# Performance work log

Measured on AMD Instinct MI355X. Metric: run time of the kernel, lower is better.

The kernel has to match this reference:

```python
import jax, jax.numpy as jnp
import numpy as np
import math

N, E, G = 10000, 100000, 500
HID, H = 128, 4
C = HID                      # out_channels per head (PyG TransformerConv)
NFREQ, NSPACE = 10, 3
EDIM = 2 * NFREQ * NSPACE    # 60 = dis_emb.dim
LAT, DIS = 6, 3
IN_DIM = HID + LAT + DIS     # 137
EPS = 1e-5


def _lin_init(k, fan_in, shape):
    b = 1.0 / math.sqrt(fan_in)
    return jax.random.uniform(k, shape, jnp.float32, -b, b)


def setup_inputs() -> dict:
    key = jax.random.key(0)
    ks = jax.random.split(key, 12)
    return dict(
        node_features=jax.random.normal(ks[0], (N, HID), jnp.float32),
        frac_coords=jax.random.uniform(ks[1], (N, DIS), jnp.float32),
        lattice_feats=jax.random.normal(ks[2], (G, LAT), jnp.float32),
        edge_index=jax.random.randint(ks[3], (2, E), 0, N),
        node2graph=jnp.sort(jax.random.randint(ks[4], (N,), 0, G)),
        frac_diff=jax.random.normal(ks[5], (E, DIS), jnp.float32) * 0.1,
        ln_gamma=jnp.ones((HID,), jnp.float32),
        ln_beta=jnp.zeros((HID,), jnp.float32),
        Wq=_lin_init(ks[6], IN_DIM, (IN_DIM, H * C)), bq=jnp.zeros((H * C,), jnp.float32),
        Wk=_lin_init(ks[7], IN_DIM, (IN_DIM, H * C)), bk=jnp.zeros((H * C,), jnp.float32),
        Wv=_lin_init(ks[8], IN_DIM, (IN_DIM, H * C)), bv=jnp.zeros((H * C,), jnp.float32),
        We=_lin_init(ks[9], EDIM, (EDIM, H * C)),
        Wskip=_lin_init(ks[10], IN_DIM, (IN_DIM, C)), bskip=jnp.zeros((C,), jnp.float32),
    )


def _sinusoids(frac_diff):
    # SinusoidsEmbedding: emb = x[...,None]*2*pi*arange(F); cat(sin, cos); detached
    freqs = 2.0 * jnp.pi * jnp.arange(NFREQ, dtype=jnp.float32)    # [F]
    emb = frac_diff[:, :, None] * freqs[None, None, :]             # [E,3,F]
    emb = emb.reshape(-1, NSPACE * NFREQ)                          # [E,30]
    return jnp.concatenate([jnp.sin(emb), jnp.cos(emb)], axis=-1)  # [E,60]


def _segment_softmax(scores, idx, num_segments):
    # softmax over variable-size neighborhoods grouped by target node idx
    m = jax.ops.segment_max(scores, idx, num_segments=num_segments)
    ex = jnp.exp(scores - m[idx])
    s = jax.ops.segment_sum(ex, idx, num_segments=num_segments)
    return ex / (s[idx] + 1e-16)


def reference(node_features, frac_coords, lattice_feats, edge_index, node2graph,
              frac_diff, ln_gamma, ln_beta, Wq, bq, Wk, bk, Wv, bv, We, Wskip, bskip):
    edge_emb = jax.lax.stop_gradient(_sinusoids(frac_diff))  # .detach() in original
    node_input = node_features
    # LayerNorm (biased variance, torch default)
    mu = node_features.mean(-1, keepdims=True)
    var = node_features.var(-1, keepdims=True)
    h = (node_features - mu) * jax.lax.rsqrt(var + EPS) * ln_gamma + ln_beta
    # gather per-graph lattice features to nodes, concat
    lat = lattice_feats.reshape(-1, LAT)[node2graph]                # [N,6]
    x = jnp.concatenate([h, lat, frac_coords], axis=1)              # [N,137]

    q = (x @ Wq + bq).reshape(N, H, C)
    k = (x @ Wk + bk).reshape(N, H, C)
    v = (x @ Wv + bv).reshape(N, H, C)
    e = (edge_emb @ We).reshape(E, H, C)                            # lin_edge (no bias)

    src, dst = edge_index[0], edge_index[1]  # message flows src -> dst (PyG default)
    k_e = k[src] + e                                                # [E,H,C]
    alpha = (q[dst] * k_e).sum(-1) / math.sqrt(C)                   # [E,H]
    alpha = _segment_softmax(alpha, dst, N)
    msg = (v[src] + e) * alpha[:, :, None]                          # [E,H,C]
    out = jax.ops.segment_sum(msg, dst, num_segments=N)             # [N,H,C]
    out = out.mean(axis=1)                                          # concat=False -> head mean
    out = out + (x @ Wskip + bskip)                                 # root skip connection
    return node_input + jax.nn.silu(out)
```

## Files before the change

kernel.cpp:

```cpp
#include <hip/hip_runtime.h>
#include <math.h>

#define N_NODES 10000
#define N_EDGES 100000
#define HIDDEN  128
#define NHEAD   4
#define CHAN    128
#define IN_DIM  137
#define KPAD    160
#define NCOLS   1904
#define NPAD    1920
#define LATD    6
#define DISD    3

#define PREP_BLOCKS 2500
#define TRANS_TILES 26
#define WQE_BLOCKS  150
#define WEBT_BLOCKS 128

#define SCAT_BLOCKS ((N_EDGES + 255) / 256)
#define GEMM_BX 15
#define GEMM_BY ((N_NODES + 63) / 64)
#define NR16    628
#define FRAG_STRIDE (5 * 64 * 8)

typedef __attribute__((ext_vector_type(8))) short short8v;
typedef __attribute__((ext_vector_type(4))) float float4v;
typedef __attribute__((ext_vector_type(2))) float float2v;

__device__ inline unsigned short f2bf(float f) {
    unsigned u = __float_as_uint(f);
    unsigned r = 0x7fffu + ((u >> 16) & 1u);
    return (unsigned short)((u + r) >> 16);
}
__device__ inline float bf2f(unsigned short u) {
    return __uint_as_float(((unsigned)u) << 16);
}
__device__ inline size_t frag_off(int grp16, int ks, int lane) {
    return (((size_t)grp16 * 5 + ks) * 64 + lane) * 8;
}
__device__ inline size_t frag_elem(int grp16, int lr, int k) {
    const int ks = k >> 5, g = (k >> 3) & 3, e = k & 7;
    return frag_off(grp16, ks, g * 16 + lr) + e;
}

__global__ __launch_bounds__(256) void prep_weights_kernel(
    const float* __restrict__ nf, const float* __restrict__ frac,
    const float* __restrict__ lat, const int* __restrict__ n2g,
    const float* __restrict__ gamma, const float* __restrict__ beta,
    const float* __restrict__ Wq, const float* __restrict__ bq,
    const float* __restrict__ Wk, const float* __restrict__ bk,
    const float* __restrict__ Wv, const float* __restrict__ bv,
    const float* __restrict__ Wsk, const float* __restrict__ bsk,
    const float* __restrict__ We,
    unsigned short* __restrict__ xfrag, int* __restrict__ hist,
    unsigned short* __restrict__ wfrag, float* __restrict__ bias_all,
    unsigned short* __restrict__ webt)
{
    __shared__ __align__(16) unsigned short Tlds[64 * 168];
    const int tid = threadIdx.x;

    if (blockIdx.x < PREP_BLOCKS) {
        int wave = tid >> 6;
        int lane = tid & 63;
        int n = blockIdx.x * 4 + wave;
        if (n >= N_NODES) return;

        float v0 = nf[n * HIDDEN + lane];
        float v1 = nf[n * HIDDEN + 64 + lane];
        float s  = v0 + v1;
        float sq = v0 * v0 + v1 * v1;
        #pragma unroll
        for (int m = 1; m < 64; m <<= 1) {
            s  += __shfl_xor(s, m);
            sq += __shfl_xor(sq, m);
        }
        float mean = s * (1.0f / 128.0f);
        float var  = sq * (1.0f / 128.0f) - mean * mean;
        float inv  = rsqrtf(var + 1e-5f);

        const int r16 = n >> 4, lr = n & 15;
        xfrag[frag_elem(r16, lr, lane)] =
            f2bf((v0 - mean) * inv * gamma[lane] + beta[lane]);
        xfrag[frag_elem(r16, lr, 64 + lane)] =
            f2bf((v1 - mean) * inv * gamma[64 + lane] + beta[64 + lane]);
        if (lane < LATD)
            xfrag[frag_elem(r16, lr, HIDDEN + lane)] = f2bf(lat[n2g[n] * LATD + lane]);
        if (lane < DISD)
            xfrag[frag_elem(r16, lr, HIDDEN + LATD + lane)] = f2bf(frac[n * DISD + lane]);
        if (lane >= 41)
            xfrag[frag_elem(r16, lr, 96 + lane)] = 0;
        if (lane == 0) hist[n] = 0;
    } else if (blockIdx.x < PREP_BLOCKS + TRANS_TILES) {
        const int n0 = (blockIdx.x - PREP_BLOCKS) * 64;
        for (int i = tid; i < 160 * 64; i += 256) {
            const int k = i >> 6, n = i & 63;
            const int col = n0 + n;
            float val = 0.0f;
            if (k < IN_DIM) {
                if (col < 512)        val = Wq[(size_t)k * 512 + col];
                else if (col < 1024)  val = Wk[(size_t)k * 512 + (col - 512)];
                else if (col < 1536)  val = Wv[(size_t)k * 512 + (col - 1024)];
                else                  val = Wsk[(size_t)k * 128 + (col - 1536)];
            }
            Tlds[n * 168 + k] = f2bf(val);
        }
        __syncthreads();
        for (int i = tid; i < 4 * 5 * 64; i += 256) {
            const int lane = i & 63;
            const int ks   = (i >> 6) % 5;
            const int c16l = i / (5 * 64);
            const int lr = lane & 15, g = lane >> 4;
            const int lcol = c16l * 16 + lr;
            const int k0 = ks * 32 + g * 8;
            const short8v v = *reinterpret_cast<const short8v*>(&Tlds[lcol * 168 + k0]);
            *reinterpret_cast<short8v*>(
                &wfrag[frag_off((n0 >> 4) + c16l, ks, lane)]) = v;
        }
        if (tid < 64) {
            const int col = n0 + tid;
            float b;
            if (col < 512)        b = bq[col];
            else if (col < 1024)  b = bk[col - 512];
            else if (col < 1536)  b = bv[col - 1024];
            else                  b = bsk[col - 1536];
            bias_all[col] = b;
        }
    } else if (blockIdx.x < PREP_BLOCKS + TRANS_TILES + WQE_BLOCKS) {
        int idx = (blockIdx.x - PREP_BLOCKS - TRANS_TILES) * 256 + tid;
        if (idx >= 240 * KPAD) return;
        int hj = idx / KPAD, k = idx % KPAD;
        int h = hj / 60, j = hj % 60;
        float s = 0.0f;
        if (k < IN_DIM) {
            #pragma unroll 4
            for (int c = 0; c < 128; ++c)
                s += Wq[(size_t)k * 512 + h * 128 + c] * We[(size_t)j * 512 + h * 128 + c];
        }
        const int col = 1664 + hj;
        wfrag[frag_elem(col >> 4, col & 15, k)] = f2bf(s);
        if (k == KPAD - 1) {
            float b = 0.0f;
            #pragma unroll 4
            for (int c = 0; c < 128; ++c)
                b += bq[h * 128 + c] * We[(size_t)j * 512 + h * 128 + c];
            bias_all[col] = b;
        }
    } else {
        int g = (blockIdx.x - PREP_BLOCKS - TRANS_TILES - WQE_BLOCKS) * 256 + tid;
        if (g >= 4 * 128 * 64) return;
        int h = g >> 13, c = (g >> 6) & 127, j = g & 63;
        float v = (j < 60) ? We[(size_t)j * 512 + h * 128 + c] : 0.0f;
        webt[g] = f2bf(v);
    }
}

__global__ __launch_bounds__(256) void hist_kernel(
    const int* __restrict__ eidx, int* __restrict__ hist)
{
    int e = blockIdx.x * 256 + threadIdx.x;
    if (e < N_EDGES) atomicAdd(&hist[eidx[N_EDGES + e]], 1);
}

__global__ __launch_bounds__(1024) void scan_kernel(
    const int* __restrict__ hist, int* __restrict__ offsets, int* __restrict__ cursor)
{
    __shared__ int part[1024];
    const int t = threadIdx.x;
    const int base = t * 10;
    int loc[10];
    int s = 0;
    #pragma unroll
    for (int i = 0; i < 10; ++i) {
        int v = (base + i < N_NODES) ? hist[base + i] : 0;
        loc[i] = s; s += v;
    }
    part[t] = s;
    __syncthreads();
    for (int off = 1; off < 1024; off <<= 1) {
        int v = (t >= off) ? part[t - off] : 0;
        __syncthreads();
        part[t] += v;
        __syncthreads();
    }
    int pre = (t > 0) ? part[t - 1] : 0;
    #pragma unroll
    for (int i = 0; i < 10; ++i)
        if (base + i < N_NODES) {
            offsets[base + i] = pre + loc[i];
            cursor[base + i]  = pre + loc[i];
        }
    if (t == 1023) offsets[N_NODES] = part[1023];
}

__global__ __launch_bounds__(256, 2) void gemm_scatter_kernel(
    const unsigned short* __restrict__ xfrag, const unsigned short* __restrict__ wfrag,
    const float* __restrict__ bias_all,
    const int* __restrict__ eidx, const float* __restrict__ fdiff,
    int* __restrict__ cursor, int* __restrict__ sorted_src,
    float* __restrict__ sorted_fd,
    float* __restrict__ sq, unsigned short* __restrict__ qbuf,
    unsigned char* __restrict__ kvb)
{
    if (blockIdx.x < SCAT_BLOCKS) {
        int e = blockIdx.x * 256 + threadIdx.x;
        if (e >= N_EDGES) return;
        int src = eidx[e];
        int dst = eidx[N_EDGES + e];
        int pos = atomicAdd(&cursor[dst], 1);
        sorted_src[pos] = src;
        sorted_fd[pos * 3 + 0] = fdiff[e * 3 + 0];
        sorted_fd[pos * 3 + 1] = fdiff[e * 3 + 1];
        sorted_fd[pos * 3 + 2] = fdiff[e * 3 + 2];
        return;
    }

    const int bx   = blockIdx.x - SCAT_BLOCKS;
    const int row0 = (bx / GEMM_BX) * 64;
    const int col0 = (bx % GEMM_BX) * 128;
    const int tid  = threadIdx.x;
    const int l    = tid & 63;
    const int wid  = tid >> 6;
    const int wr   = (wid >> 1) * 32;
    const int wc   = (wid & 1) * 64;
    const int lr   = l & 15;
    const int r16  = (row0 + wr) >> 4;
    const int c16  = (col0 + wc) >> 4;

    short8v a[2][5], b[4][5];
    #pragma unroll
    for (int ks = 0; ks < 5; ++ks) {
        #pragma unroll
        for (int t = 0; t < 2; ++t)
            a[t][ks] = *reinterpret_cast<const short8v*>(
                &xfrag[frag_off(r16 + t, ks, l)]);
        #pragma unroll
        for (int t = 0; t < 4; ++t)
            b[t][ks] = *reinterpret_cast<const short8v*>(
                &wfrag[frag_off(c16 + t, ks, l)]);
    }

    float4v acc[2][4];
    #pragma unroll
    for (int tr = 0; tr < 2; ++tr)
        #pragma unroll
        for (int tc = 0; tc < 4; ++tc)
            acc[tr][tc] = (float4v){0.0f, 0.0f, 0.0f, 0.0f};

    #pragma unroll
    for (int ks = 0; ks < 5; ++ks)
        #pragma unroll
        for (int tr = 0; tr < 2; ++tr)
            #pragma unroll
            for (int tc = 0; tc < 4; ++tc)
                acc[tr][tc] = __builtin_amdgcn_mfma_f32_16x16x32_bf16(
                    a[tr][ks], b[tc][ks], acc[tr][tc], 0, 0, 0);

    #pragma unroll
    for (int tr = 0; tr < 2; ++tr) {
        #pragma unroll
        for (int tc = 0; tc < 4; ++tc) {
            const int col  = col0 + wc + tc * 16 + lr;
            const float bias = bias_all[col];
            #pragma unroll
            for (int j = 0; j < 4; ++j) {
                const int row = row0 + wr + tr * 16 + (l >> 4) * 4 + j;
                if (row < N_NODES) {
                    float val = acc[tr][tc][j] + bias;
                    if (col < 512) {
                        qbuf[(size_t)row * 512 + col] = f2bf(val);
                    } else if (col < 1024) {
                        const int h = (col - 512) >> 7, ck = (col - 512) & 127;
                        int p = __builtin_amdgcn_cvt_pk_fp8_f32(val, val, 0, false);
                        kvb[((size_t)row * 4 + h) * 256 + ck] = (unsigned char)(p & 0xFF);
                    } else if (col < 1536) {
                        const int h = (col - 1024) >> 7, cv = (col - 1024) & 127;
                        int p = __builtin_amdgcn_cvt_pk_fp8_f32(val, val, 0, false);
                        kvb[((size_t)row * 4 + h) * 256 + 128 + cv] = (unsigned char)(p & 0xFF);
                    } else if (col < 1664) {
                        sq[(size_t)row * 384 + (col - 1536)] = val;
                    } else if (col < NCOLS) {
                        sq[(size_t)row * 384 + 128 + (col - 1664)] = val;
                    }
                }
            }
        }
    }
}

__global__ __launch_bounds__(256) void gather_kernel(
    const float* __restrict__ sq, const unsigned short* __restrict__ qbuf,
    const unsigned char* __restrict__ kvb,
    const int* __restrict__ offsets, const int* __restrict__ sorted_src,
    const float* __restrict__ sorted_fd,
    float* __restrict__ avbuf, unsigned short* __restrict__ aggbuf,
    float* __restrict__ sumwbuf)
{
    const int n    = blockIdx.x;
    const int h    = threadIdx.x >> 6;
    const int l    = threadIdx.x & 63;
    const int hl   = l & 31;
    const int half = l >> 5;
    const float TWO_PI = 6.283185307179586f;
    const float scale  = 0.08838834764831845f;

    const ushort4 qv = *reinterpret_cast<const ushort4*>(
        &qbuf[(size_t)n * 512 + h * 128 + 4 * hl]);
    const float q4x = bf2f(qv.x), q4y = bf2f(qv.y);
    const float q4z = bf2f(qv.z), q4w = bf2f(qv.w);
    const float qe_a = sq[(size_t)n * 384 + 128 + h * 60 + hl];
    const bool  v2ok = (hl < 28);
    const float qe_b = v2ok ? sq[(size_t)n * 384 + 128 + h * 60 + hl + 32] : 0.0f;

    const int   jj1  = (hl < 30) ? hl : hl - 30;
    const int   sd1  = jj1 / 10;
    const float fc1  = TWO_PI * (float)(jj1 % 10);
    const bool  sin1 = (hl < 30);
    const int   jj2  = hl + 2;
    const int   sd2  = v2ok ? (jj2 / 10) : 0;
    const float fc2  = v2ok ? TWO_PI * (float)(jj2 % 10) : 0.0f;

    float ax = 0.f, ay = 0.f, az = 0.f, aw = 0.f;
    float agg1 = 0.f, agg2 = 0.f, sumw = 0.f;
    const int e0 = offsets[n], e1 = offsets[n + 1];

    for (int base = e0; base < e1; base += 4) {
        const int eA = base + half;
        const int eB = base + half + 2;
        const bool okA = (eA < e1), okB = (eB < e1);
        const int iA = okA ? eA : e0;
        const int iB = okB ? eB : e0;
        const int srcA = sorted_src[iA];
        const int srcB = sorted_src[iB];
        const float fdA1 = sorted_fd[iA * 3 + sd1];
        const float fdA2 = sorted_fd[iA * 3 + sd2];
        const float fdB1 = sorted_fd[iB * 3 + sd1];
        const float fdB2 = sorted_fd[iB * 3 + sd2];
        const unsigned char* pA = kvb + ((size_t)srcA * 4 + h) * 256;
        const unsigned char* pB = kvb + ((size_t)srcB * 4 + h) * 256;
        const unsigned kAu = *reinterpret_cast<const unsigned*>(pA + 4 * hl);
        const unsigned vAu = *reinterpret_cast<const unsigned*>(pA + 128 + 4 * hl);
        const unsigned kBu = *reinterpret_cast<const unsigned*>(pB + 4 * hl);
        const unsigned vBu = *reinterpret_cast<const unsigned*>(pB + 128 + 4 * hl);

        const float eA1 = sin1 ? __sinf(fdA1 * fc1) : __cosf(fdA1 * fc1);
        const float eA2 = __cosf(fdA2 * fc2);
        const float eB1 = sin1 ? __sinf(fdB1 * fc1) : __cosf(fdB1 * fc1);
        const float eB2 = __cosf(fdB2 * fc2);

        const float2v kA01 = __builtin_amdgcn_cvt_pk_f32_fp8(kAu, false);
        const float2v kA23 = __builtin_amdgcn_cvt_pk_f32_fp8(kAu, true);
        const float2v kB01 = __builtin_amdgcn_cvt_pk_f32_fp8(kBu, false);
        const float2v kB23 = __builtin_amdgcn_cvt_pk_f32_fp8(kBu, true);

        float pAs = q4x * kA01[0] + q4y * kA01[1]
                  + q4z * kA23[0] + q4w * kA23[1]
                  + eA1 * qe_a + eA2 * qe_b;
        float pBs = q4x * kB01[0] + q4y * kB01[1]
                  + q4z * kB23[0] + q4w * kB23[1]
                  + eB1 * qe_a + eB2 * qe_b;
        #pragma unroll
        for (int m = 1; m <= 16; m <<= 1) {
            pAs += __shfl_xor(pAs, m);
            pBs += __shfl_xor(pBs, m);
        }
        const float wA = okA ? __expf(pAs * scale) : 0.0f;
        const float wB = okB ? __expf(pBs * scale) : 0.0f;
        sumw += wA + wB;

        const float2v vA01 = __builtin_amdgcn_cvt_pk_f32_fp8(vAu, false);
        const float2v vA23 = __builtin_amdgcn_cvt_pk_f32_fp8(vAu, true);
        const float2v vB01 = __builtin_amdgcn_cvt_pk_f32_fp8(vBu, false);
        const float2v vB23 = __builtin_amdgcn_cvt_pk_f32_fp8(vBu, true);
        ax += wA * vA01[0] + wB * vB01[0];
        ay += wA * vA01[1] + wB * vB01[1];
        az += wA * vA23[0] + wB * vB23[0];
        aw += wA * vA23[1] + wB * vB23[1];
        agg1 += wA * eA1 + wB * eB1;
        if (v2ok) agg2 += wA * eA2 + wB * eB2;
    }

    sumw += __shfl_xor(sumw, 32);
    ax += __shfl_xor(ax, 32);  ay += __shfl_xor(ay, 32);
    az += __shfl_xor(az, 32);  aw += __shfl_xor(aw, 32);
    agg1 += __shfl_xor(agg1, 32);
    agg2 += __shfl_xor(agg2, 32);

    if (half == 0) {
        float4 r;
        r.x = ax; r.y = ay; r.z = az; r.w = aw;
        *reinterpret_cast<float4*>(&avbuf[(size_t)n * 512 + h * 128 + 4 * hl]) = r;
        aggbuf[n * 256 + h * 64 + hl]      = f2bf(agg1);
        aggbuf[n * 256 + h * 64 + 32 + hl] = f2bf(agg2);
        if (hl == 0) sumwbuf[n * 4 + h] = sumw;
    }
}

__global__ __launch_bounds__(256) void corrfin_kernel(
    const unsigned short* __restrict__ webt, const unsigned short* __restrict__ aggbuf,
    const float* __restrict__ avbuf, const float* __restrict__ sumwbuf,
    const float* __restrict__ sq, const float* __restrict__ nf,
    float* __restrict__ out)
{
    const int node0 = blockIdx.x * 64;
    const int tid = threadIdx.x;
    const int l   = tid & 63;
    const int w   = tid >> 6;
    const int lr  = l & 15;
    const int lk  = (l >> 4) * 8;
    const int nbase = node0 + w * 16;

    float4v acc[4][8];
    #pragma unroll
    for (int h = 0; h < 4; ++h)
        #pragma unroll
        for (int nn = 0; nn < 8; ++nn)
            acc[h][nn] = (float4v){0.0f, 0.0f, 0.0f, 0.0f};

    const int arow = (nbase + lr < N_NODES) ? (nbase + lr) : 0;
    #pragma unroll
    for (int h = 0; h < 4; ++h) {
        #pragma unroll
        for (int ks = 0; ks < 2; ++ks) {
            const short8v a = *reinterpret_cast<const short8v*>(
                &aggbuf[(size_t)arow * 256 + h * 64 + ks * 32 + lk]);
            #pragma unroll
            for (int nn = 0; nn < 8; ++nn) {
                const short8v b = *reinterpret_cast<const short8v*>(
                    &webt[(size_t)(h * 128 + nn * 16 + lr) * 64 + ks * 32 + lk]);
                acc[h][nn] = __builtin_amdgcn_mfma_f32_16x16x32_bf16(a, b, acc[h][nn], 0, 0, 0);
            }
        }
    }

    float inv_sw[4][4];
    #pragma unroll
    for (int j = 0; j < 4; ++j) {
        const int node = nbase + (l >> 4) * 4 + j;
        const int nrd  = (node < N_NODES) ? node : 0;
        #pragma unroll
        for (int h = 0; h < 4; ++h)
            inv_sw[j][h] = 1.0f / (sumwbuf[nrd * 4 + h] + 1e-16f);
    }

    #pragma unroll
    for (int nn = 0; nn < 8; ++nn) {
        const int col = nn * 16 + lr;
        #pragma unroll
        for (int j = 0; j < 4; ++j) {
            const int node = nbase + (l >> 4) * 4 + j;
            if (node < N_NODES) {
                float z = 0.0f;
                #pragma unroll
                for (int h = 0; h < 4; ++h)
                    z += (avbuf[(size_t)node * 512 + h * 128 + col] + acc[h][nn][j])
                         * inv_sw[j][h];
                z = 0.25f * z + sq[(size_t)node * 384 + col];
                float si = z / (1.0f + __expf(-z));
                out[node * CHAN + col] = nf[node * CHAN + col] + si;
            }
        }
    }
}

extern "C" void kernel_launch(void* const* d_in, const int* in_sizes, int n_in,
                              void* d_out, int out_size, void* d_ws, size_t ws_size,
                              hipStream_t stream)
{
    const float* nf    = (const float*)d_in[0];
    const float* frac  = (const float*)d_in[1];
    const float* lat   = (const float*)d_in[2];
    const int*   eidx  = (const int*)  d_in[3];
    const int*   n2g   = (const int*)  d_in[4];
    const float* fdiff = (const float*)d_in[5];
    const float* gamma = (const float*)d_in[6];
    const float* beta  = (const float*)d_in[7];
    const float* Wq    = (const float*)d_in[8];
    const float* bq    = (const float*)d_in[9];
    const float* Wk    = (const float*)d_in[10];
    const float* bk    = (const float*)d_in[11];
    const float* Wv    = (const float*)d_in[12];
    const float* bv    = (const float*)d_in[13];
    const float* We    = (const float*)d_in[14];
    const float* Wsk   = (const float*)d_in[15];
    const float* bsk   = (const float*)d_in[16];
    float* out = (float*)d_out;

    float* sq        = (float*)d_ws;
    float* avbuf     = sq + (size_t)N_NODES * 384;
    float* sumwbuf   = avbuf + (size_t)N_NODES * 512;
    float* bias_all  = sumwbuf + (size_t)N_NODES * 4;
    float* sorted_fd = bias_all + NPAD;
    unsigned short* xfrag  = (unsigned short*)(sorted_fd + (size_t)N_EDGES * 3);
    unsigned short* wfrag  = xfrag + (size_t)NR16 * FRAG_STRIDE;
    unsigned short* webt   = wfrag + (size_t)(NPAD / 16) * FRAG_STRIDE;
    unsigned short* aggbuf = webt + 4 * 128 * 64;
    unsigned short* qbuf   = aggbuf + (size_t)N_NODES * 256;
    unsigned char*  kvb    = (unsigned char*)(qbuf + (size_t)N_NODES * 512);
    int* hist       = (int*)(kvb + (size_t)N_NODES * 4 * 256);
    int* offsets    = hist + N_NODES;
    int* cursor     = offsets + N_NODES + 1;
    int* sorted_src = cursor + N_NODES;

    prep_weights_kernel<<<PREP_BLOCKS + TRANS_TILES + WQE_BLOCKS + WEBT_BLOCKS,
                          256, 0, stream>>>(
        nf, frac, lat, n2g, gamma, beta,
        Wq, bq, Wk, bk, Wv, bv, Wsk, bsk, We,
        xfrag, hist, wfrag, bias_all, webt);

    hist_kernel<<<(N_EDGES + 255) / 256, 256, 0, stream>>>(eidx, hist);
    scan_kernel<<<1, 1024, 0, stream>>>(hist, offsets, cursor);

    gemm_scatter_kernel<<<SCAT_BLOCKS + GEMM_BX * GEMM_BY, 256, 0, stream>>>(
        xfrag, wfrag, bias_all, eidx, fdiff, cursor, sorted_src, sorted_fd,
        sq, qbuf, kvb);

    gather_kernel<<<N_NODES, 256, 0, stream>>>(
        sq, qbuf, kvb, offsets, sorted_src, sorted_fd, avbuf, aggbuf, sumwbuf);

    corrfin_kernel<<<(N_NODES + 63) / 64, 256, 0, stream>>>(
        webt, aggbuf, avbuf, sumwbuf, sq, nf, out);
}
```

Before: 130.2 us.

## Fuse hist and scan via last-block pattern, bf16 avbuf, lower GEMM register use

Merges the histogram and prefix-scan kernels into one launch: the last block to finish, detected with an atomic done-counter, performs the scan. This removes a kernel launch and the single-block 1024-thread scan gap. The gather output avbuf is stored as bf16 instead of fp32 to halve its write and read traffic, which adds some rounding error. The GEMM now loads B fragments per k-step instead of all upfront and raises launch bounds to 4 blocks per CU for more occupancy.

```diff
diff --git a/kernel.cpp b/kernel.cpp
--- a/kernel.cpp
+++ b/kernel.cpp
@@ -54,6 +54,7 @@
     const float* __restrict__ Wsk, const float* __restrict__ bsk,
     const float* __restrict__ We,
     unsigned short* __restrict__ xfrag, int* __restrict__ hist,
+    int* __restrict__ donecnt,
     unsigned short* __restrict__ wfrag, float* __restrict__ bias_all,
     unsigned short* __restrict__ webt)
 {
@@ -61,6 +62,7 @@
     const int tid = threadIdx.x;
 
     if (blockIdx.x < PREP_BLOCKS) {
+        if (blockIdx.x == 0 && tid == 0) *donecnt = 0;
         int wave = tid >> 6;
         int lane = tid & 63;
         int n = blockIdx.x * 4 + wave;
@@ -155,45 +157,53 @@
     }
 }
 
-__global__ __launch_bounds__(256) void hist_kernel(
-    const int* __restrict__ eidx, int* __restrict__ hist)
+__global__ __launch_bounds__(256) void histscan_kernel(
+    const int* __restrict__ eidx, int* __restrict__ hist, int* __restrict__ donecnt,
+    int* __restrict__ offsets, int* __restrict__ cursor)
 {
-    int e = blockIdx.x * 256 + threadIdx.x;
+    const int t = threadIdx.x;
+    int e = blockIdx.x * 256 + t;
     if (e < N_EDGES) atomicAdd(&hist[eidx[N_EDGES + e]], 1);
-}
-
-__global__ __launch_bounds__(1024) void scan_kernel(
-    const int* __restrict__ hist, int* __restrict__ offsets, int* __restrict__ cursor)
-{
-    __shared__ int part[1024];
-    const int t = threadIdx.x;
-    const int base = t * 10;
-    int loc[10];
+    __threadfence();
+    __syncthreads();
+    __shared__ int isLast;
+    if (t == 0)
+        isLast = (atomicAdd(donecnt, 1) == (int)gridDim.x - 1);
+    __syncthreads();
+    if (!isLast) return;
+
+    __shared__ int part[256];
+    const int base = t * 40;
     int s = 0;
-    #pragma unroll
-    for (int i = 0; i < 10; ++i) {
-        int v = (base + i < N_NODES) ? hist[base + i] : 0;
-        loc[i] = s; s += v;
+    for (int i = 0; i < 40; ++i) {
+        int idx = base + i;
+        int v = (idx < N_NODES)
+            ? __hip_atomic_load(&hist[idx], __ATOMIC_RELAXED, __HIP_MEMORY_SCOPE_AGENT)
+            : 0;
+        s += v;
     }
     part[t] = s;
     __syncthreads();
-    for (int off = 1; off < 1024; off <<= 1) {
+    for (int off = 1; off < 256; off <<= 1) {
         int v = (t >= off) ? part[t - off] : 0;
         __syncthreads();
         part[t] += v;
         __syncthreads();
     }
-    int pre = (t > 0) ? part[t - 1] : 0;
-    #pragma unroll
-    for (int i = 0; i < 10; ++i)
-        if (base + i < N_NODES) {
-            offsets[base + i] = pre + loc[i];
-            cursor[base + i]  = pre + loc[i];
-        }
-    if (t == 1023) offsets[N_NODES] = part[1023];
-}
-
-__global__ __launch_bounds__(256, 2) void gemm_scatter_kernel(
+    int run = (t > 0) ? part[t - 1] : 0;
+    for (int i = 0; i < 40; ++i) {
+        int idx = base + i;
+        if (idx < N_NODES) {
+            int v = __hip_atomic_load(&hist[idx], __ATOMIC_RELAXED, __HIP_MEMORY_SCOPE_AGENT);
+            offsets[idx] = run;
+            cursor[idx]  = run;
+            run += v;
+        }
+    }
+    if (t == 255) offsets[N_NODES] = part[255];
+}
+
+__global__ __launch_bounds__(256, 4) void gemm_scatter_kernel(
     const unsigned short* __restrict__ xfrag, const unsigned short* __restrict__ wfrag,
     const float* __restrict__ bias_all,
     const int* __restrict__ eidx, const float* __restrict__ fdiff,
@@ -227,18 +237,13 @@
     const int r16  = (row0 + wr) >> 4;
     const int c16  = (col0 + wc) >> 4;
 
-    short8v a[2][5], b[4][5];
-    #pragma unroll
-    for (int ks = 0; ks < 5; ++ks) {
+    short8v a[2][5];
+    #pragma unroll
+    for (int ks = 0; ks < 5; ++ks)
         #pragma unroll
         for (int t = 0; t < 2; ++t)
             a[t][ks] = *reinterpret_cast<const short8v*>(
                 &xfrag[frag_off(r16 + t, ks, l)]);
-        #pragma unroll
-        for (int t = 0; t < 4; ++t)
-            b[t][ks] = *reinterpret_cast<const short8v*>(
-                &wfrag[frag_off(c16 + t, ks, l)]);
-    }
 
     float4v acc[2][4];
     #pragma unroll
@@ -248,13 +253,19 @@
             acc[tr][tc] = (float4v){0.0f, 0.0f, 0.0f, 0.0f};
 
     #pragma unroll
-    for (int ks = 0; ks < 5; ++ks)
+    for (int ks = 0; ks < 5; ++ks) {
+        short8v b[4];
+        #pragma unroll
+        for (int t = 0; t < 4; ++t)
+            b[t] = *reinterpret_cast<const short8v*>(
+                &wfrag[frag_off(c16 + t, ks, l)]);
         #pragma unroll
         for (int tr = 0; tr < 2; ++tr)
             #pragma unroll
             for (int tc = 0; tc < 4; ++tc)
                 acc[tr][tc] = __builtin_amdgcn_mfma_f32_16x16x32_bf16(
-                    a[tr][ks], b[tc][ks], acc[tr][tc], 0, 0, 0);
+                    a[tr][ks], b[tc], acc[tr][tc], 0, 0, 0);
+    }
 
     #pragma unroll
     for (int tr = 0; tr < 2; ++tr) {
@@ -293,7 +304,7 @@
     const unsigned char* __restrict__ kvb,
     const int* __restrict__ offsets, const int* __restrict__ sorted_src,
     const float* __restrict__ sorted_fd,
-    float* __restrict__ avbuf, unsigned short* __restrict__ aggbuf,
+    unsigned short* __restrict__ avbh, unsigned short* __restrict__ aggbuf,
     float* __restrict__ sumwbuf)
 {
     const int n    = blockIdx.x;
@@ -387,9 +398,9 @@
     agg2 += __shfl_xor(agg2, 32);
 
     if (half == 0) {
-        float4 r;
-        r.x = ax; r.y = ay; r.z = az; r.w = aw;
-        *reinterpret_cast<float4*>(&avbuf[(size_t)n * 512 + h * 128 + 4 * hl]) = r;
+        ushort4 r;
+        r.x = f2bf(ax); r.y = f2bf(ay); r.z = f2bf(az); r.w = f2bf(aw);
+        *reinterpret_cast<ushort4*>(&avbh[(size_t)n * 512 + h * 128 + 4 * hl]) = r;
         aggbuf[n * 256 + h * 64 + hl]      = f2bf(agg1);
         aggbuf[n * 256 + h * 64 + 32 + hl] = f2bf(agg2);
         if (hl == 0) sumwbuf[n * 4 + h] = sumw;
@@ -398,7 +409,7 @@
 
 __global__ __launch_bounds__(256) void corrfin_kernel(
     const unsigned short* __restrict__ webt, const unsigned short* __restrict__ aggbuf,
-    const float* __restrict__ avbuf, const float* __restrict__ sumwbuf,
+    const unsigned short* __restrict__ avbh, const float* __restrict__ sumwbuf,
     const float* __restrict__ sq, const float* __restrict__ nf,
     float* __restrict__ out)
 {
@@ -453,7 +464,7 @@
                 float z = 0.0f;
                 #pragma unroll
                 for (int h = 0; h < 4; ++h)
-                    z += (avbuf[(size_t)node * 512 + h * 128 + col] + acc[h][nn][j])
+                    z += (bf2f(avbh[(size_t)node * 512 + h * 128 + col]) + acc[h][nn][j])
                          * inv_sw[j][h];
                 z = 0.25f * z + sq[(size_t)node * 384 + col];
                 float si = z / (1.0f + __expf(-z));
@@ -487,8 +498,7 @@
     float* out = (float*)d_out;
 
     float* sq        = (float*)d_ws;
-    float* avbuf     = sq + (size_t)N_NODES * 384;
-    float* sumwbuf   = avbuf + (size_t)N_NODES * 512;
+    float* sumwbuf   = sq + (size_t)N_NODES * 384;
     float* bias_all  = sumwbuf + (size_t)N_NODES * 4;
     float* sorted_fd = bias_all + NPAD;
     unsigned short* xfrag  = (unsigned short*)(sorted_fd + (size_t)N_EDGES * 3);
@@ -496,9 +506,11 @@
     unsigned short* webt   = wfrag + (size_t)(NPAD / 16) * FRAG_STRIDE;
     unsigned short* aggbuf = webt + 4 * 128 * 64;
     unsigned short* qbuf   = aggbuf + (size_t)N_NODES * 256;
-    unsigned char*  kvb    = (unsigned char*)(qbuf + (size_t)N_NODES * 512);
+    unsigned short* avbh   = qbuf + (size_t)N_NODES * 512;
+    unsigned char*  kvb    = (unsigned char*)(avbh + (size_t)N_NODES * 512);
     int* hist       = (int*)(kvb + (size_t)N_NODES * 4 * 256);
-    int* offsets    = hist + N_NODES;
+    int* donecnt    = hist + N_NODES;
+    int* offsets    = donecnt + 1;
     int* cursor     = offsets + N_NODES + 1;
     int* sorted_src = cursor + N_NODES;
 
@@ -506,18 +518,18 @@
                           256, 0, stream>>>(
         nf, frac, lat, n2g, gamma, beta,
         Wq, bq, Wk, bk, Wv, bv, Wsk, bsk, We,
-        xfrag, hist, wfrag, bias_all, webt);
-
-    hist_kernel<<<(N_EDGES + 255) / 256, 256, 0, stream>>>(eidx, hist);
-    scan_kernel<<<1, 1024, 0, stream>>>(hist, offsets, cursor);
+        xfrag, hist, donecnt, wfrag, bias_all, webt);
+
+    histscan_kernel<<<SCAT_BLOCKS, 256, 0, stream>>>(
+        eidx, hist, donecnt, offsets, cursor);
 
     gemm_scatter_kernel<<<SCAT_BLOCKS + GEMM_BX * GEMM_BY, 256, 0, stream>>>(
         xfrag, wfrag, bias_all, eidx, fdiff, cursor, sorted_src, sorted_fd,
         sq, qbuf, kvb);
 
     gather_kernel<<<N_NODES, 256, 0, stream>>>(
-        sq, qbuf, kvb, offsets, sorted_src, sorted_fd, avbuf, aggbuf, sumwbuf);
+        sq, qbuf, kvb, offsets, sorted_src, sorted_fd, avbh, aggbuf, sumwbuf);
 
     corrfin_kernel<<<(N_NODES + 63) / 64, 256, 0, stream>>>(
-        webt, aggbuf, avbuf, sumwbuf, sq, nf, out);
-}
+        webt, aggbuf, avbh, sumwbuf, sq, nf, out);
+}
```

Result: slower. 161.9 us (+24.3%).
